# Performance work log

Hardware: AMD Instinct MI355X
Metric: run time of the kernel (lower is better)

The kernel has to match this reference:

```python
import jax, jax.numpy as jnp
import numpy as np

CLIPS_NUM = 4
OUTPUT_SIZE = 1000000  # outputSize: number of features in trainset (scales Z)
T = 0.07               # temperature
QUEUE_K = 131072       # queue size
D = 128                # inputSize (feature dim)
BS = 256               # batch_size * clips_num


def _l2norm(x):
    return x / jnp.linalg.norm(x, axis=-1, keepdims=True)


def setup_inputs() -> dict:
    key = jax.random.key(0)
    kq, kk, km = jax.random.split(key, 3)
    # MoCo-style L2-normalized features keep exp(sim/T) finite.
    q = _l2norm(jax.random.normal(kq, (BS, D), jnp.float32))
    k = _l2norm(jax.random.normal(kk, (BS, D), jnp.float32))
    memory = _l2norm(jax.random.normal(km, (QUEUE_K, D), jnp.float32))
    return {"q": q, "k": k, "memory": memory, "i": 0}


def _make_indices(bs, clips_num):
    """Static (numpy) replication of MemoryMoCo.prepare_indices."""
    batch_size = bs // clips_num
    # indices[v] = row indices of all clips of video v: [batch_size, clips_num]
    indices = np.arange(bs).reshape(clips_num, batch_size).T
    vid = np.arange(bs) % batch_size
    all_clips = vid[:, None] + np.arange(clips_num)[None, :] * batch_size  # [bs, clips_num]
    mask = all_clips != np.arange(bs)[:, None]
    pos_indices = all_clips[mask].reshape(bs, clips_num - 1)  # drop self
    return jnp.asarray(indices), jnp.asarray(pos_indices)


def reference(q, k, memory, i):
    bs, d = q.shape
    batch_size = bs // CLIPS_NUM
    indices, pos_indices = _make_indices(bs, CLIPS_NUM)

    k = jax.lax.stop_gradient(k)            # k = k.detach()
    mem = jax.lax.stop_gradient(memory)     # queue = memory.clone().detach()

    # l_pos: gather positives, per-row bmm with q, mean over positives -> [bs, 1]
    positives = k[pos_indices]              # [bs, clips_num-1, d]
    l_pos = jnp.mean(jnp.einsum('bpd,bd->bp', positives, q), axis=-1, keepdims=True)

    # l_neg: queue GEMM -> [bs, K]
    l_neg = q @ mem.T

    out = jnp.concatenate([l_pos, l_neg], axis=1)   # [bs, 1+K]
    out = jnp.exp(out / T)
    # First-call NCE normalization: Z = out.mean() * outputSize (Z is detached in torch)
    Z = jax.lax.stop_gradient(jnp.mean(out) * OUTPUT_SIZE)
    out = out / Z

    probs = jnp.mean(out[:, 0] / jnp.sum(out, axis=1))  # extract_probs

    # no_grad memory-bank update: scatter mean of each video's clip keys
    out_ids = jnp.arange(batch_size) % memory.shape[0]   # index=0, fmod queueSize
    k_mean = jnp.mean(k[indices], axis=1)                # [batch_size, d]
    new_memory = memory.at[out_ids].set(k_mean)

    return out, probs, new_memory
```

## Files before the change

### kernel.cpp

```cpp
#include <hip/hip_runtime.h>
#include <hip/hip_bf16.h>

constexpr int       DIM       = 128;
constexpr long long CN        = 131073;
constexpr long long OUT_ELEMS = 256LL * 131073LL;
constexpr long long PROBS_OFF = OUT_ELEMS;
constexpr long long MEMOUT_OFF = OUT_ELEMS + 1;
constexpr long long MEM_ELEMS = 131072LL * 128LL;

constexpr float SCL = 20.60992915555662f;

constexpr int WS_INVZ  = 0;
constexpr int WS_ELPOS = 16;
constexpr int WS_KMEAN = 272;
constexpr int WS_ROWP  = 8464;
constexpr int WS_QB    = 16656;

typedef __attribute__((ext_vector_type(8))) short  short8v;
typedef __attribute__((ext_vector_type(4))) float  f32x4;

__device__ __forceinline__ unsigned short f2bf(float x) {
  unsigned u = __float_as_uint(x);
  u += 0x7fffu + ((u >> 16) & 1u);
  return (unsigned short)(u >> 16);
}

__global__ void k_init(float* __restrict__ ws) {
  int i = blockIdx.x * 256 + threadIdx.x;
  if (i < 32 * 256) ws[WS_ROWP + i] = 0.f;
}

__global__ void k_prep(const float* __restrict__ q, const float* __restrict__ k,
                       float* __restrict__ ws) {
  int b = blockIdx.x, t = threadIdx.x;
  if (b < 128) {
    int i = b * 256 + t;
    unsigned short* qb = (unsigned short*)(ws + WS_QB);
    qb[i] = f2bf(q[i]);
  } else if (b < 160) {
    int j = (b - 128) * 256 + t;
    int v = j >> 7, d = j & 127;
    ws[WS_KMEAN + j] = 0.25f * (k[v*128+d] + k[(v+64)*128+d] +
                                k[(v+128)*128+d] + k[(v+192)*128+d]);
  } else {
    int row = t, vid = t & 63;
    float acc = 0.f;
    for (int d = 0; d < DIM; ++d) {
      float s = 0.f;
      #pragma unroll
      for (int c = 0; c < 4; ++c) {
        int rr = vid + c * 64;
        if (rr != row) s += k[rr*128 + d];
      }
      acc += q[row*128 + d] * s;
    }
    ws[WS_ELPOS + row] = exp2f(acc * (1.f/3.f) * SCL);
  }
}

template<int PASS>
__global__ __launch_bounds__(256) void k_gemm(const float* __restrict__ memv,
                                              float* __restrict__ ws,
                                              float* __restrict__ out) {
  __shared__ __align__(16) char lds[8192];
  const int t = threadIdx.x;
  const int n0 = blockIdx.x * 32;
  float invZ = 1.f;
  if (PASS == 1) invZ = ws[WS_INVZ];

  {
    const float4* src = (const float4*)(memv + (long long)n0 * DIM);
    #pragma unroll
    for (int j = 0; j < 4; ++j) {
      int fi4 = t + j * 256;
      float4 v = src[fi4];
      int fi = fi4 * 4;
      int n = fi >> 7;
      int byteoff = (fi * 2) ^ ((n & 7) << 4);
      ushort4 h;
      h.x = f2bf(v.x); h.y = f2bf(v.y); h.z = f2bf(v.z); h.w = f2bf(v.w);
      *(ushort4*)(lds + byteoff) = h;
    }
  }
  __syncthreads();

  const int lane = t & 63, wave = t >> 6;
  const int g = lane >> 4, nlo = lane & 15;
  f32x4 zero = {0.f, 0.f, 0.f, 0.f};
  f32x4 acc[4][2];
  #pragma unroll
  for (int mf = 0; mf < 4; ++mf) { acc[mf][0] = zero; acc[mf][1] = zero; }

  const char* qb = (const char*)(ws + WS_QB);
  #pragma unroll
  for (int ks = 0; ks < 4; ++ks) {
    short8v bfr[2];
    #pragma unroll
    for (int nf = 0; nf < 2; ++nf) {
      int n = nf * 16 + nlo;
      int byteoff = (n * 256 + ks * 64 + g * 16) ^ ((n & 7) << 4);
      bfr[nf] = *(const short8v*)(lds + byteoff);
    }
    #pragma unroll
    for (int mf = 0; mf < 4; ++mf) {
      int m = wave * 64 + mf * 16 + nlo;
      short8v af = *(const short8v*)(qb + (m * 128 + ks * 32 + g * 8) * 2);
      acc[mf][0] = __builtin_amdgcn_mfma_f32_16x16x32_bf16(af, bfr[0], acc[mf][0], 0, 0, 0);
      acc[mf][1] = __builtin_amdgcn_mfma_f32_16x16x32_bf16(af, bfr[1], acc[mf][1], 0, 0, 0);
    }
  }

  float* rowp = ws + WS_ROWP + (blockIdx.x & 31) * 256;
  #pragma unroll
  for (int mf = 0; mf < 4; ++mf) {
    #pragma unroll
    for (int r = 0; r < 4; ++r) {
      int row = wave * 64 + mf * 16 + g * 4 + r;
      float v0 = exp2f(acc[mf][0][r] * SCL);
      float v1 = exp2f(acc[mf][1][r] * SCL);
      if (PASS == 0) {
        float part = v0 + v1;
        part += __shfl_xor(part, 1, 16);
        part += __shfl_xor(part, 2, 16);
        part += __shfl_xor(part, 4, 16);
        part += __shfl_xor(part, 8, 16);
        if (nlo == 0) atomicAdd(&rowp[row], part);
      } else {
        long long base = (long long)row * CN + 1 + n0;
        out[base + nlo]      = v0 * invZ;
        out[base + 16 + nlo] = v1 * invZ;
      }
    }
  }
}

__global__ void k_fin(float* __restrict__ ws, float* __restrict__ out) {
  __shared__ float s_tot[256];
  __shared__ float s_pr[256];
  __shared__ float sh_invZ;
  int t = threadIdx.x;
  float s = ws[WS_ELPOS + t];
  float rs = s;
  for (int sl = 0; sl < 32; ++sl) rs += ws[WS_ROWP + sl * 256 + t];
  s_tot[t] = rs;
  s_pr[t] = s / rs;
  __syncthreads();
  for (int off = 128; off > 0; off >>= 1) {
    if (t < off) { s_tot[t] += s_tot[t + off]; s_pr[t] += s_pr[t + off]; }
    __syncthreads();
  }
  if (t == 0) {
    double Z = (double)s_tot[0] * (1000000.0 / (256.0 * 131073.0));
    float invZ = (float)(1.0 / Z);
    ws[WS_INVZ] = invZ;
    sh_invZ = invZ;
    out[PROBS_OFF] = s_pr[0] * (1.f / 256.f);
  }
  __syncthreads();
  out[(long long)t * CN] = s * sh_invZ;
}

__global__ void k_copy(const float* __restrict__ memv, const float* __restrict__ ws,
                       float* __restrict__ out) {
  float* dst = out + MEMOUT_OFF;
  const float* km = ws + WS_KMEAN;
  long long gid = blockIdx.x * 256LL + threadIdx.x;
  if (gid == 0) {
    dst[0] = km[0]; dst[1] = km[1]; dst[2] = km[2];
    dst[MEM_ELEMS - 1] = memv[MEM_ELEMS - 1];
  }
  const long long ng = (MEM_ELEMS - 4) / 4;
  long long stride = (long long)gridDim.x * 256LL;
  for (long long i = gid; i < ng; i += stride) {
    long long base = 3 + i * 4;
    float4 v;
    if (base + 4 <= 8192) {
      v.x = km[base]; v.y = km[base+1]; v.z = km[base+2]; v.w = km[base+3];
    } else if (base >= 8192) {
      v.x = memv[base]; v.y = memv[base+1]; v.z = memv[base+2]; v.w = memv[base+3];
    } else {
      float tmp[4];
      #pragma unroll
      for (int e = 0; e < 4; ++e) {
        long long idx = base + e;
        tmp[e] = (idx < 8192) ? km[idx] : memv[idx];
      }
      v.x = tmp[0]; v.y = tmp[1]; v.z = tmp[2]; v.w = tmp[3];
    }
    *(float4*)(dst + base) = v;
  }
}

extern "C" void kernel_launch(void* const* d_in, const int* in_sizes, int n_in,
                              void* d_out, int out_size, void* d_ws, size_t ws_size,
                              hipStream_t stream) {
  (void)in_sizes; (void)n_in; (void)out_size; (void)ws_size;
  const float* q    = (const float*)d_in[0];
  const float* k    = (const float*)d_in[1];
  const float* memv = (const float*)d_in[2];
  float* out = (float*)d_out;
  float* ws  = (float*)d_ws;

  hipLaunchKernelGGL(k_init, dim3(32),   dim3(256), 0, stream, ws);
  hipLaunchKernelGGL(k_prep, dim3(161),  dim3(256), 0, stream, q, k, ws);
  hipLaunchKernelGGL((k_gemm<0>), dim3(4096), dim3(256), 0, stream, memv, ws, out);
  hipLaunchKernelGGL(k_fin,  dim3(1),    dim3(256), 0, stream, ws, out);
  hipLaunchKernelGGL((k_gemm<1>), dim3(4096), dim3(256), 0, stream, memv, ws, out);
  hipLaunchKernelGGL(k_copy, dim3(2048), dim3(256), 0, stream, memv, ws, out);
}
```

Baseline: 462.3 us.

## Pre-convert memory bank to bf16 once and use persistent GEMM tiles with register-held Q

The memory bank is converted to bf16 once in the prep kernel into workspace, so both GEMM passes read half the bytes and skip the per-block conversion and LDS staging. The GEMM kernels now loop over several column tiles per block, keeping the Q fragments in registers and accumulating row sums locally before a single atomic per row. The separate init kernel is folded into prep, and the l_pos computation is parallelised across waves with shuffle reductions. The trade-off is an extra 32 MB bf16 write and read of the bank, plus B fragments loaded straight from global memory with no LDS reuse.

New measurement: 399.8 us. 13.5% less time.

```diff
diff --git a/kernel.cpp b/kernel.cpp
--- a/kernel.cpp
+++ b/kernel.cpp
@@ -1,12 +1,12 @@
 #include <hip/hip_runtime.h>
 #include <hip/hip_bf16.h>
 
-constexpr int       DIM       = 128;
-constexpr long long CN        = 131073;
-constexpr long long OUT_ELEMS = 256LL * 131073LL;
-constexpr long long PROBS_OFF = OUT_ELEMS;
+constexpr int       DIM        = 128;
+constexpr long long CN         = 131073;
+constexpr long long OUT_ELEMS  = 256LL * 131073LL;
+constexpr long long PROBS_OFF  = OUT_ELEMS;
 constexpr long long MEMOUT_OFF = OUT_ELEMS + 1;
-constexpr long long MEM_ELEMS = 131072LL * 128LL;
+constexpr long long MEM_ELEMS  = 131072LL * 128LL;
 
 constexpr float SCL = 20.60992915555662f;
 
@@ -15,6 +15,13 @@
 constexpr int WS_KMEAN = 272;
 constexpr int WS_ROWP  = 8464;
 constexpr int WS_QB    = 16656;
+constexpr int WS_MEMBF = 33040;
+
+constexpr int PB_Q    = 8192;
+constexpr int PB_KM   = 8208;
+constexpr int PB_LPOS = 8240;
+constexpr int PB_ZERO = 8304;
+constexpr int PREP_BLOCKS = 8308;
 
 typedef __attribute__((ext_vector_type(8))) short  short8v;
 typedef __attribute__((ext_vector_type(4))) float  f32x4;
@@ -25,110 +32,135 @@
   return (unsigned short)(u >> 16);
 }
 
-__global__ void k_init(float* __restrict__ ws) {
-  int i = blockIdx.x * 256 + threadIdx.x;
-  if (i < 32 * 256) ws[WS_ROWP + i] = 0.f;
-}
-
-__global__ void k_prep(const float* __restrict__ q, const float* __restrict__ k,
-                       float* __restrict__ ws) {
-  int b = blockIdx.x, t = threadIdx.x;
-  if (b < 128) {
-    int i = b * 256 + t;
-    unsigned short* qb = (unsigned short*)(ws + WS_QB);
-    qb[i] = f2bf(q[i]);
-  } else if (b < 160) {
-    int j = (b - 128) * 256 + t;
+__device__ __forceinline__ short8v pack8(float4 a, float4 b) {
+  short8v h;
+  h[0] = (short)f2bf(a.x); h[1] = (short)f2bf(a.y);
+  h[2] = (short)f2bf(a.z); h[3] = (short)f2bf(a.w);
+  h[4] = (short)f2bf(b.x); h[5] = (short)f2bf(b.y);
+  h[6] = (short)f2bf(b.z); h[7] = (short)f2bf(b.w);
+  return h;
+}
+
+__global__ __launch_bounds__(256) void k_prep(const float* __restrict__ q,
+                                              const float* __restrict__ k,
+                                              const float* __restrict__ memv,
+                                              float* __restrict__ ws) {
+  const int b = blockIdx.x, t = threadIdx.x;
+  if (b < PB_Q) {
+    long long gid = (long long)b * 256 + t;
+    const float4* src = (const float4*)memv;
+    float4 a = src[2 * gid], c = src[2 * gid + 1];
+    short8v* dst = (short8v*)((unsigned short*)(ws + WS_MEMBF) + gid * 8);
+    *dst = pack8(a, c);
+  } else if (b < PB_KM) {
+    int gid = (b - PB_Q) * 256 + t;
+    const float4* src = (const float4*)q;
+    float4 a = src[2 * gid], c = src[2 * gid + 1];
+    short8v* dst = (short8v*)((unsigned short*)(ws + WS_QB) + gid * 8);
+    *dst = pack8(a, c);
+  } else if (b < PB_LPOS) {
+    int j = (b - PB_KM) * 256 + t;
     int v = j >> 7, d = j & 127;
     ws[WS_KMEAN + j] = 0.25f * (k[v*128+d] + k[(v+64)*128+d] +
                                 k[(v+128)*128+d] + k[(v+192)*128+d]);
+  } else if (b < PB_ZERO) {
+    int row = (b - PB_LPOS) * 4 + (t >> 6);
+    int lane = t & 63;
+    int vid = row & 63;
+    float2 qv = ((const float2*)(q + row * DIM))[lane];
+    float2 kr = ((const float2*)(k + row * DIM))[lane];
+    float s0 = -kr.x, s1 = -kr.y;
+    #pragma unroll
+    for (int c = 0; c < 4; ++c) {
+      float2 kc = ((const float2*)(k + (vid + c * 64) * DIM))[lane];
+      s0 += kc.x; s1 += kc.y;
+    }
+    float acc = qv.x * s0 + qv.y * s1;
+    #pragma unroll
+    for (int off = 1; off < 64; off <<= 1) acc += __shfl_xor(acc, off, 64);
+    if (lane == 0) ws[WS_ELPOS + row] = exp2f(acc * (1.f / 3.f) * SCL);
   } else {
-    int row = t, vid = t & 63;
-    float acc = 0.f;
-    for (int d = 0; d < DIM; ++d) {
-      float s = 0.f;
-      #pragma unroll
-      for (int c = 0; c < 4; ++c) {
-        int rr = vid + c * 64;
-        if (rr != row) s += k[rr*128 + d];
-      }
-      acc += q[row*128 + d] * s;
-    }
-    ws[WS_ELPOS + row] = exp2f(acc * (1.f/3.f) * SCL);
-  }
-}
-
-template<int PASS>
-__global__ __launch_bounds__(256) void k_gemm(const float* __restrict__ memv,
+    int i = (b - PB_ZERO) * 2048 + t * 8;
+    float4 z = {0.f, 0.f, 0.f, 0.f};
+    *(float4*)(ws + WS_ROWP + i)     = z;
+    *(float4*)(ws + WS_ROWP + i + 4) = z;
+  }
+}
+
+template<int PASS, int NT, int GRID>
+__global__ __launch_bounds__(256) void k_gemm(const unsigned short* __restrict__ membf,
+                                              const unsigned short* __restrict__ qb,
                                               float* __restrict__ ws,
                                               float* __restrict__ out) {
-  __shared__ __align__(16) char lds[8192];
-  const int t = threadIdx.x;
-  const int n0 = blockIdx.x * 32;
-  float invZ = 1.f;
+  const int t = threadIdx.x, lane = t & 63, wave = t >> 6;
+  const int g = lane >> 4, nlo = lane & 15;
+  float invZ = 0.f;
   if (PASS == 1) invZ = ws[WS_INVZ];
 
-  {
-    const float4* src = (const float4*)(memv + (long long)n0 * DIM);
-    #pragma unroll
-    for (int j = 0; j < 4; ++j) {
-      int fi4 = t + j * 256;
-      float4 v = src[fi4];
-      int fi = fi4 * 4;
-      int n = fi >> 7;
-      int byteoff = (fi * 2) ^ ((n & 7) << 4);
-      ushort4 h;
-      h.x = f2bf(v.x); h.y = f2bf(v.y); h.z = f2bf(v.z); h.w = f2bf(v.w);
-      *(ushort4*)(lds + byteoff) = h;
-    }
-  }
-  __syncthreads();
-
-  const int lane = t & 63, wave = t >> 6;
-  const int g = lane >> 4, nlo = lane & 15;
-  f32x4 zero = {0.f, 0.f, 0.f, 0.f};
-  f32x4 acc[4][2];
+  short8v af[4][4];
   #pragma unroll
-  for (int mf = 0; mf < 4; ++mf) { acc[mf][0] = zero; acc[mf][1] = zero; }
-
-  const char* qb = (const char*)(ws + WS_QB);
-  #pragma unroll
-  for (int ks = 0; ks < 4; ++ks) {
-    short8v bfr[2];
-    #pragma unroll
-    for (int nf = 0; nf < 2; ++nf) {
-      int n = nf * 16 + nlo;
-      int byteoff = (n * 256 + ks * 64 + g * 16) ^ ((n & 7) << 4);
-      bfr[nf] = *(const short8v*)(lds + byteoff);
-    }
+  for (int ks = 0; ks < 4; ++ks)
+    #pragma unroll
+    for (int mf = 0; mf < 4; ++mf)
+      af[ks][mf] = *(const short8v*)(qb + (wave*64 + mf*16 + nlo) * DIM + ks*32 + g*8);
+
+  float sums[4][4];
+  if (PASS == 0) {
+    #pragma unroll
+    for (int mf = 0; mf < 4; ++mf)
+      #pragma unroll
+      for (int r = 0; r < 4; ++r) sums[mf][r] = 0.f;
+  }
+
+  for (int it = 0; it < NT; ++it) {
+    const int tile = blockIdx.x + it * GRID;
+    const long long n0 = (long long)tile * 32;
+    f32x4 acc[4][2];
+    f32x4 zero = {0.f, 0.f, 0.f, 0.f};
+    #pragma unroll
+    for (int mf = 0; mf < 4; ++mf) { acc[mf][0] = zero; acc[mf][1] = zero; }
+
+    #pragma unroll
+    for (int ks = 0; ks < 4; ++ks) {
+      short8v b0 = *(const short8v*)(membf + (n0 + nlo)      * DIM + ks*32 + g*8);
+      short8v b1 = *(const short8v*)(membf + (n0 + 16 + nlo) * DIM + ks*32 + g*8);
+      #pragma unroll
+      for (int mf = 0; mf < 4; ++mf) {
+        acc[mf][0] = __builtin_amdgcn_mfma_f32_16x16x32_bf16(af[ks][mf], b0, acc[mf][0], 0, 0, 0);
+        acc[mf][1] = __builtin_amdgcn_mfma_f32_16x16x32_bf16(af[ks][mf], b1, acc[mf][1], 0, 0, 0);
+      }
+    }
+
     #pragma unroll
     for (int mf = 0; mf < 4; ++mf) {
-      int m = wave * 64 + mf * 16 + nlo;
-      short8v af = *(const short8v*)(qb + (m * 128 + ks * 32 + g * 8) * 2);
-      acc[mf][0] = __builtin_amdgcn_mfma_f32_16x16x32_bf16(af, bfr[0], acc[mf][0], 0, 0, 0);
-      acc[mf][1] = __builtin_amdgcn_mfma_f32_16x16x32_bf16(af, bfr[1], acc[mf][1], 0, 0, 0);
-    }
-  }
-
-  float* rowp = ws + WS_ROWP + (blockIdx.x & 31) * 256;
-  #pragma unroll
-  for (int mf = 0; mf < 4; ++mf) {
-    #pragma unroll
-    for (int r = 0; r < 4; ++r) {
-      int row = wave * 64 + mf * 16 + g * 4 + r;
-      float v0 = exp2f(acc[mf][0][r] * SCL);
-      float v1 = exp2f(acc[mf][1][r] * SCL);
-      if (PASS == 0) {
-        float part = v0 + v1;
-        part += __shfl_xor(part, 1, 16);
-        part += __shfl_xor(part, 2, 16);
-        part += __shfl_xor(part, 4, 16);
-        part += __shfl_xor(part, 8, 16);
-        if (nlo == 0) atomicAdd(&rowp[row], part);
-      } else {
-        long long base = (long long)row * CN + 1 + n0;
-        out[base + nlo]      = v0 * invZ;
-        out[base + 16 + nlo] = v1 * invZ;
+      #pragma unroll
+      for (int r = 0; r < 4; ++r) {
+        float v0 = exp2f(acc[mf][0][r] * SCL);
+        float v1 = exp2f(acc[mf][1][r] * SCL);
+        if (PASS == 0) {
+          sums[mf][r] += v0 + v1;
+        } else {
+          int row = wave*64 + mf*16 + g*4 + r;
+          long long base = (long long)row * CN + 1 + n0;
+          out[base + nlo]      = v0 * invZ;
+          out[base + 16 + nlo] = v1 * invZ;
+        }
+      }
+    }
+  }
+
+  if (PASS == 0) {
+    float* rowp = ws + WS_ROWP + (blockIdx.x & 31) * 256;
+    #pragma unroll
+    for (int mf = 0; mf < 4; ++mf) {
+      #pragma unroll
+      for (int r = 0; r < 4; ++r) {
+        float s = sums[mf][r];
+        s += __shfl_xor(s, 1, 16);
+        s += __shfl_xor(s, 2, 16);
+        s += __shfl_xor(s, 4, 16);
+        s += __shfl_xor(s, 8, 16);
+        if (nlo == 0) atomicAdd(&rowp[wave*64 + mf*16 + g*4 + r], s);
       }
     }
   }
@@ -200,11 +232,12 @@
   const float* memv = (const float*)d_in[2];
   float* out = (float*)d_out;
   float* ws  = (float*)d_ws;
-
-  hipLaunchKernelGGL(k_init, dim3(32),   dim3(256), 0, stream, ws);
-  hipLaunchKernelGGL(k_prep, dim3(161),  dim3(256), 0, stream, q, k, ws);
-  hipLaunchKernelGGL((k_gemm<0>), dim3(4096), dim3(256), 0, stream, memv, ws, out);
+  const unsigned short* membf = (const unsigned short*)(ws + WS_MEMBF);
+  const unsigned short* qb    = (const unsigned short*)(ws + WS_QB);
+
+  hipLaunchKernelGGL(k_prep, dim3(PREP_BLOCKS), dim3(256), 0, stream, q, k, memv, ws);
+  hipLaunchKernelGGL((k_gemm<0, 8, 512>),  dim3(512),  dim3(256), 0, stream, membf, qb, ws, out);
   hipLaunchKernelGGL(k_fin,  dim3(1),    dim3(256), 0, stream, ws, out);
-  hipLaunchKernelGGL((k_gemm<1>), dim3(4096), dim3(256), 0, stream, memv, ws, out);
+  hipLaunchKernelGGL((k_gemm<1, 4, 1024>), dim3(1024), dim3(256), 0, stream, membf, qb, ws, out);
   hipLaunchKernelGGL(k_copy, dim3(2048), dim3(256), 0, stream, memv, ws, out);
 }
```
